# Kernel optimization log

Hardware: AMD Instinct MI355X
Metric: run time of the kernel (lower is better)

Reference implementation:

```python
import jax, jax.numpy as jnp
import numpy as np

B, S, HID = 2, 2048, 2048
H, DN, DR, KVR, DV = 16, 128, 64, 512, 128
THETA = 10000.0
EPS = 1e-6
SCALE = (DN + DR) ** -0.5  # softmax_scale = q_head_dim ** -0.5 (rope_scaling is None)


def setup_inputs() -> dict:
    key = jax.random.key(0)
    ks = jax.random.split(key, 8)
    std = 0.02
    return {
        "hidden_states": jax.random.normal(ks[0], (B, S, HID), jnp.float32),
        "q_nope_weight": jax.random.normal(ks[1], (H * DN, HID), jnp.float32) * std,
        "q_pe_weight": jax.random.normal(ks[2], (H * DR, HID), jnp.float32) * std,
        "kv_a_weight": jax.random.normal(ks[3], (KVR + DR, HID), jnp.float32) * std,
        "kv_a_ln_weight": jnp.ones((KVR,), jnp.float32),
        "k_b_weight": jax.random.normal(ks[4], (H, DN, KVR), jnp.float32) * std,
        "v_b_weight": jax.random.normal(ks[5], (H, DV, KVR), jnp.float32) * std,
        "o_weight": jax.random.normal(ks[6], (HID, H * DV), jnp.float32) * std,
        "position_ids": jnp.arange(S, dtype=jnp.int32)[None, :],
    }


def _rotate_half(x):
    x1, x2 = jnp.split(x, 2, axis=-1)
    return jnp.concatenate((-x2, x1), axis=-1)


def _interleave(x):
    # torch: x.view(..., d//2, 2).transpose(-1, -2).reshape(..., d)
    *lead, d = x.shape
    x = x.reshape(*lead, d // 2, 2)
    x = jnp.swapaxes(x, -1, -2)
    return x.reshape(*lead, d)


def reference(hidden_states, q_nope_weight, q_pe_weight, kv_a_weight,
              kv_a_ln_weight, k_b_weight, v_b_weight, o_weight, position_ids):
    b, s, _ = hidden_states.shape
    # Q projections, split into no-rope and rope parts per head
    q_nope = jnp.einsum('bsh,ndh->bnsd', hidden_states, q_nope_weight.reshape(H, DN, HID))
    q_pe = jnp.einsum('bsh,ndh->bnsd', hidden_states, q_pe_weight.reshape(H, DR, HID))
    # Joint low-rank KV + shared rope-key projection (MQA-style)
    ckv_kpe = jnp.einsum('bsh,ch->bsc', hidden_states, kv_a_weight)  # [b,s,KVR+DR]
    ckv, k_pe = ckv_kpe[..., :KVR], ckv_kpe[..., KVR:]
    # RMSNorm over the compressed latent (kv_a_layernorm)
    var = jnp.mean(jnp.square(ckv), axis=-1, keepdims=True)
    ckv = ckv * jax.lax.rsqrt(var + EPS) * kv_a_ln_weight  # [b,s,KVR]
    # Rotary tables: cos/sin indexed by position_ids, broadcast over heads
    inv_freq = 1.0 / (THETA ** (jnp.arange(0, DR, 2, dtype=jnp.float32) / DR))
    t = position_ids.astype(jnp.float32)                 # [1,s]
    freqs = t[..., None] * inv_freq                      # [1,s,DR/2]
    emb = jnp.concatenate((freqs, freqs), axis=-1)       # [1,s,DR]
    cos = jnp.cos(emb)[:, None]                          # [1,1,s,DR]
    sin = jnp.sin(emb)[:, None]
    # Partial RoPE with the interleave permutation from apply_rotary_pos_emb
    q_pe = _interleave(q_pe)
    k_pe = _interleave(k_pe[:, None])                    # [b,1,s,DR]
    q_pe = q_pe * cos + _rotate_half(q_pe) * sin
    k_pe = (k_pe * cos + _rotate_half(k_pe) * sin)[:, 0] # [b,s,DR]
    # Weight absorption: fold k_b into q, attend directly in the latent space
    q_lat = jnp.einsum('bnsd,ndc->bnsc', q_nope, k_b_weight)  # [b,H,s,KVR]
    scores = (jnp.einsum('bnsc,btc->bnst', q_lat, ckv)
              + jnp.einsum('bnsd,btd->bnst', q_pe, k_pe)) * SCALE
    mask = jnp.tril(jnp.ones((s, s), dtype=bool))
    scores = jnp.where(mask, scores, jnp.finfo(scores.dtype).min)
    attn = jax.nn.softmax(scores, axis=-1)
    # Attention output in the latent space, then expand with v_b and o_proj
    out_lat = jnp.einsum('bnst,btc->bnsc', attn, ckv)         # [b,H,s,KVR]
    v_out = jnp.einsum('bnsc,ndc->bnsd', out_lat, v_b_weight) # [b,H,s,DV]
    v_out = v_out.transpose(0, 2, 1, 3).reshape(b, s, H * DV)
    return jnp.einsum('bsf,hf->bsh', v_out, o_weight)
```

## Files before the change

### kernel.cpp

```cpp
#include <hip/hip_runtime.h>
#include <hip/hip_bf16.h>


typedef __hip_bfloat16 bf16;
typedef __bf16 v8bf __attribute__((ext_vector_type(8)));
typedef float  v4f  __attribute__((ext_vector_type(4)));

#define S_    2048
#define SCALE_F 0.07216878364870322f

__device__ __forceinline__ void st1(float* p, float v){ *p = v; }
__device__ __forceinline__ void st1(bf16* p, float v){ *p = __float2bfloat16(v); }
__device__ __forceinline__ unsigned short bfb(float x){
  return __builtin_bit_cast(unsigned short, __float2bfloat16(x));
}
__device__ __forceinline__ unsigned pk2(float a, float b){
  return (unsigned)bfb(a) | ((unsigned)bfb(b) << 16);
}

typedef const void __attribute__((address_space(1)))* gas_t;
typedef void __attribute__((address_space(3)))* las_t;
__device__ __forceinline__ void g2l16(const void* g, void* l){
  __builtin_amdgcn_global_load_lds((gas_t)g, (las_t)l, 16, 0, 0);
}

__global__ void cossin_kernel(const int* __restrict__ pos, float* __restrict__ cosT,
                              float* __restrict__ sinT){
  int idx = blockIdx.x*256 + threadIdx.x;
  int i = idx & 31, s = idx >> 5;
  float t = (float)pos[s];
  float freq = t * powf(10000.0f, -(float)i/32.0f);
  cosT[idx] = cosf(freq);
  sinT[idx] = sinf(freq);
}

__global__ void castf2b_kernel(const float* __restrict__ src, bf16* __restrict__ dst, int n8){
  int i = blockIdx.x*256 + threadIdx.x;
  if (i >= n8) return;
  const float4* s = (const float4*)src;
  float4 a = s[2*i], b = s[2*i+1];
  uint4 o; o.x = pk2(a.x,a.y); o.y = pk2(a.z,a.w); o.z = pk2(b.x,b.y); o.w = pk2(b.z,b.w);
  ((uint4*)dst)[i] = o;
}

template<typename TC>
__global__ __launch_bounds__(256) void gemm2_kernel(
    const bf16* __restrict__ A, int lda, int aDiv, long aS1, long aS2,
    const bf16* __restrict__ W, int ldw, int wDiv, long wS1, long wS2,
    TC* __restrict__ C, int ldc, int cDiv, long cS1, long cS2,
    int N, int K, float alpha)
{
  int z = blockIdx.z;
  A += (long)(z/aDiv)*aS1 + (long)(z%aDiv)*aS2;
  W += (long)(z/wDiv)*wS1 + (long)(z%wDiv)*wS2;
  C += (long)(z/cDiv)*cS1 + (long)(z%cDiv)*cS2;
  __shared__ bf16 As[2][4096];
  __shared__ bf16 Ws[2][4096];
  const int tid = threadIdx.x;
  const int w = tid>>6, l = tid&63, g = l>>4, c16 = l&15;
  const int wr = (w>>1)*64, wc = (w&1)*64;
  const int row0 = blockIdx.y*128, col0 = blockIdx.x*128;

  const long aO1 = (long)(row0 + (tid>>2))*lda + (tid&3)*8;
  const long aO2 = (long)(row0 + 64 + (tid>>2))*lda + (tid&3)*8;
  int wr1 = col0 + (tid>>2);      if (wr1 > N-1) wr1 = N-1;
  int wr2 = col0 + 64 + (tid>>2); if (wr2 > N-1) wr2 = N-1;
  const long wO1 = (long)wr1*ldw + (tid&3)*8;
  const long wO2 = (long)wr2*ldw + (tid&3)*8;

  v4f acc[4][4];
  #pragma unroll
  for (int i=0;i<4;i++)
    #pragma unroll
    for (int j=0;j<4;j++) acc[i][j] = (v4f){0.f,0.f,0.f,0.f};

  auto STAGE = [&](int k0, int bsel){
    g2l16(A + aO1 + k0, &As[bsel][tid*8]);
    g2l16(A + aO2 + k0, &As[bsel][2048 + tid*8]);
    g2l16(W + wO1 + k0, &Ws[bsel][tid*8]);
    g2l16(W + wO2 + k0, &Ws[bsel][2048 + tid*8]);
  };
  STAGE(0, 0);
  __syncthreads();
  const int nk = K >> 5;
  for (int t=0; t<nk; ++t){
    const int cur = t & 1;
    if (t+1 < nk) STAGE((t+1)*32, cur^1);
    v8bf af[4], bw[4];
    #pragma unroll
    for (int mi=0;mi<4;mi++) af[mi] = *(const v8bf*)&As[cur][(wr+mi*16+c16)*32 + g*8];
    #pragma unroll
    for (int ni=0;ni<4;ni++) bw[ni] = *(const v8bf*)&Ws[cur][(wc+ni*16+c16)*32 + g*8];
    #pragma unroll
    for (int mi=0;mi<4;mi++)
      #pragma unroll
      for (int ni=0;ni<4;ni++)
        acc[mi][ni] = __builtin_amdgcn_mfma_f32_16x16x32_bf16(af[mi], bw[ni], acc[mi][ni], 0,0,0);
    __syncthreads();
  }
  #pragma unroll
  for (int mi=0;mi<4;mi++)
    #pragma unroll
    for (int ni=0;ni<4;ni++)
      #pragma unroll
      for (int r=0;r<4;r++){
        int row = row0 + wr + mi*16 + g*4 + r;
        int col = col0 + wc + ni*16 + c16;
        if (col < N) st1(C + (long)row*ldc + col, acc[mi][ni][r]*alpha);
      }
}

__global__ __launch_bounds__(256) void proj3_kernel(
    const bf16* __restrict__ A,
    const bf16* __restrict__ Wq, const bf16* __restrict__ Wp, const bf16* __restrict__ Wc,
    bf16* __restrict__ Cq, bf16* __restrict__ Cp, bf16* __restrict__ Cc)
{
  const int bx = blockIdx.x;
  const bf16* W; bf16* C; int ldc, N, col0;
  if (bx < 16){ W = Wq; C = Cq; ldc = 2048; N = 2048; col0 = bx*128; }
  else if (bx < 24){ W = Wp; C = Cp; ldc = 1024; N = 1024; col0 = (bx-16)*128; }
  else { W = Wc; C = Cc; ldc = 576; N = 576; col0 = (bx-24)*128; }
  __shared__ bf16 As[2][4096];
  __shared__ bf16 Ws[2][4096];
  const int tid = threadIdx.x;
  const int w = tid>>6, l = tid&63, g = l>>4, c16 = l&15;
  const int wr = (w>>1)*64, wc = (w&1)*64;
  const int row0 = blockIdx.y*128;

  const long aO1 = (long)(row0 + (tid>>2))*2048 + (tid&3)*8;
  const long aO2 = (long)(row0 + 64 + (tid>>2))*2048 + (tid&3)*8;
  int wr1 = col0 + (tid>>2);      if (wr1 > N-1) wr1 = N-1;
  int wr2 = col0 + 64 + (tid>>2); if (wr2 > N-1) wr2 = N-1;
  const long wO1 = (long)wr1*2048 + (tid&3)*8;
  const long wO2 = (long)wr2*2048 + (tid&3)*8;

  v4f acc[4][4];
  #pragma unroll
  for (int i=0;i<4;i++)
    #pragma unroll
    for (int j=0;j<4;j++) acc[i][j] = (v4f){0.f,0.f,0.f,0.f};

  auto STAGE = [&](int k0, int bsel){
    g2l16(A + aO1 + k0, &As[bsel][tid*8]);
    g2l16(A + aO2 + k0, &As[bsel][2048 + tid*8]);
    g2l16(W + wO1 + k0, &Ws[bsel][tid*8]);
    g2l16(W + wO2 + k0, &Ws[bsel][2048 + tid*8]);
  };
  STAGE(0, 0);
  __syncthreads();
  for (int t=0; t<64; ++t){
    const int cur = t & 1;
    if (t+1 < 64) STAGE((t+1)*32, cur^1);
    v8bf af[4], bw[4];
    #pragma unroll
    for (int mi=0;mi<4;mi++) af[mi] = *(const v8bf*)&As[cur][(wr+mi*16+c16)*32 + g*8];
    #pragma unroll
    for (int ni=0;ni<4;ni++) bw[ni] = *(const v8bf*)&Ws[cur][(wc+ni*16+c16)*32 + g*8];
    #pragma unroll
    for (int mi=0;mi<4;mi++)
      #pragma unroll
      for (int ni=0;ni<4;ni++)
        acc[mi][ni] = __builtin_amdgcn_mfma_f32_16x16x32_bf16(af[mi], bw[ni], acc[mi][ni], 0,0,0);
    __syncthreads();
  }
  #pragma unroll
  for (int mi=0;mi<4;mi++)
    #pragma unroll
    for (int ni=0;ni<4;ni++)
      #pragma unroll
      for (int r=0;r<4;r++){
        int row = row0 + wr + mi*16 + g*4 + r;
        int col = col0 + wc + ni*16 + c16;
        if (col < N) C[(long)row*ldc + col] = __float2bfloat16(acc[mi][ni][r]);
      }
}

__global__ __launch_bounds__(256) void kbT_kernel(const float* __restrict__ kb,
                                                  bf16* __restrict__ kbT){
  __shared__ bf16 t[64][65];
  int h = blockIdx.z, c0 = blockIdx.x*64, d0 = blockIdx.y*64;
  const float* src = kb + ((long)h*128 + d0)*512 + c0;
  #pragma unroll
  for (int i=0;i<16;i++){
    int idx = i*256 + threadIdx.x;
    int dl = idx>>6, cl = idx&63;
    t[dl][cl] = __float2bfloat16(src[(long)dl*512 + cl]);
  }
  __syncthreads();
  bf16* dst = kbT + ((long)h*512 + c0)*128 + d0;
  #pragma unroll
  for (int i=0;i<16;i++){
    int idx = i*256 + threadIdx.x;
    int cl = idx>>6, dl = idx&63;
    dst[(long)cl*128 + dl] = t[dl][cl];
  }
}

__global__ __launch_bounds__(256) void tposeV_kernel(const bf16* __restrict__ Kb,
                                                     bf16* __restrict__ Kd){
  __shared__ bf16 t[64][65];
  int b = blockIdx.z, s0 = blockIdx.y*64, d0 = blockIdx.x*64;
  const bf16* src = Kb + ((long)(b*S_ + s0))*576 + d0;
  #pragma unroll
  for (int i=0;i<16;i++){
    int idx = i*256 + threadIdx.x;
    int sl = idx>>6, dl = idx&63;
    t[sl][dl] = src[(long)sl*576 + dl];
  }
  __syncthreads();
  bf16* dst = Kd + ((long)(b*512 + d0))*S_ + s0;
  #pragma unroll
  for (int i=0;i<16;i++){
    int idx = i*256 + threadIdx.x;
    int dl = idx>>6, sl = idx&63;
    dst[(long)dl*S_ + sl] = t[sl][dl];
  }
}

__global__ __launch_bounds__(256) void build_k_kernel(
    const bf16* __restrict__ ckv_kpe, const float* __restrict__ ln_w,
    const float* __restrict__ cosT, const float* __restrict__ sinT,
    bf16* __restrict__ Kb)
{
  int row = blockIdx.x;
  int s = row & (S_-1);
  int tid = threadIdx.x;
  const bf16* src = ckv_kpe + (long)row*576;
  float x0 = __bfloat162float(src[tid*2]), x1 = __bfloat162float(src[tid*2+1]);
  float ss = x0*x0 + x1*x1;
  #pragma unroll
  for (int o=32;o>=1;o>>=1) ss += __shfl_xor(ss, o, 64);
  __shared__ float wss[4];
  int wid = tid>>6, lane = tid&63;
  if (lane==0) wss[wid] = ss;
  __syncthreads();
  float tot = wss[0]+wss[1]+wss[2]+wss[3];
  float rs = rsqrtf(tot*(1.0f/512.0f) + 1e-6f);
  bf16* dst = Kb + (long)row*576;
  dst[tid*2]   = __float2bfloat16(x0*rs*ln_w[tid*2]);
  dst[tid*2+1] = __float2bfloat16(x1*rs*ln_w[tid*2+1]);
  if (tid < 32) {
    float p0 = __bfloat162float(src[512 + tid*2]);
    float p1 = __bfloat162float(src[512 + tid*2 + 1]);
    float c = cosT[s*32+tid], sn = sinT[s*32+tid];
    dst[512+tid] = __float2bfloat16(p0*c - p1*sn);
    dst[544+tid] = __float2bfloat16(p1*c + p0*sn);
  }
}

__global__ void rope_q_kernel(const bf16* __restrict__ qpe,
                              const float* __restrict__ cosT, const float* __restrict__ sinT,
                              bf16* __restrict__ Qb)
{
  int idx = blockIdx.x*256 + threadIdx.x;
  int i = idx & 31;
  int s = (idx >> 5) & (S_-1);
  int z = idx >> 16;
  int b = z >> 4, n = z & 15;
  long base = ((long)(b*S_+s))*1024 + n*64 + 2*i;
  float x0 = __bfloat162float(qpe[base]), x1 = __bfloat162float(qpe[base+1]);
  float c = cosT[s*32+i], sn = sinT[s*32+i];
  bf16* dst = Qb + ((long)z*S_ + s)*576;
  dst[512+i] = __float2bfloat16((x0*c - x1*sn)*SCALE_F);
  dst[544+i] = __float2bfloat16((x1*c + x0*sn)*SCALE_F);
}

#define K0_OFF 0
#define K1_OFF 36864
#define V0_OFF 73728
#define V1_OFF 106496
#define SX_OFF 139264
#define P_OFF  147456
#define SMEM_BYTES 152576

__global__ __launch_bounds__(512, 2) void attn_mfma_kernel(
    const bf16* __restrict__ Qg, const bf16* __restrict__ Kg,
    const bf16* __restrict__ Vdg, bf16* __restrict__ Og)
{
  extern __shared__ char smem[];
  const int tid = threadIdx.x;
  const int w   = tid >> 6;
  const int l   = tid & 63;
  const int g   = l >> 4;
  const int c16 = l & 15;
  const int rg  = w & 3;
  const int dh  = w >> 2;
  const int R   = rg * 16;
  const int Dh  = dh * 256;
  const int DQb = dh * 576;
  char* SX = smem + SX_OFF + rg*2048;
  char* Pp = smem + P_OFF  + rg*1280;

  const int lin = blockIdx.x;
  const int k8 = lin & 7;
  const int b  = k8 >> 2;
  const int u  = (lin >> 3)*4 + (k8 & 3);
  const int n  = u & 15;
  const int pr = u >> 4;
  const int z  = b*16 + n;

  const char* kb0 = (const char*)Kg  + (long)b*S_*1152;
  const char* vd0 = (const char*)Vdg + (long)b*512*S_*2;

  int kOffG[5], kOffL[5], vOffG[4], vOffL[4];
  #pragma unroll
  for (int it=0; it<4; it++){
    int c = it*512 + tid;
    int kcol = c/72, j = c - kcol*72;
    kOffG[it] = kcol*1152 + ((j ^ (kcol&7))<<4);
    kOffL[it] = c*16;
  }
  {
    int c = 2048 + tid;
    int kcol = c/72, j = c - kcol*72;
    kOffG[4] = kcol*1152 + ((j ^ (kcol&7))<<4);
    kOffL[4] = c*16;
  }
  #pragma unroll
  for (int it=0; it<4; it++){
    int c = it*512 + tid;
    int s = c>>3, uu = (c&7) ^ (s&7);
    int d = 2*s + (uu>>2), j = uu&3;
    vOffG[it] = d*(S_*2) + j*16;
    vOffL[it] = c*16;
  }

  auto STAGE = [&](int tt, char* kd, char* vd){
    const char* ksrc = kb0 + (long)tt*36864;
    #pragma unroll
    for (int it=0; it<4; it++) g2l16(ksrc + kOffG[it], kd + kOffL[it]);
    if (tid < 256) g2l16(ksrc + kOffG[4], kd + kOffL[4]);
    const char* vsrc = vd0 + (long)tt*64;
    #pragma unroll
    for (int it=0; it<4; it++) g2l16(vsrc + vOffG[it], vd + vOffL[it]);
  };

  for (int ph = 0; ph < 2; ++ph){
    const int qt = ph ? (31 - pr) : pr;
    const int q0 = qt * 64;

    v8bf qf[9];
    {
      const char* qgb = (const char*)Qg + ((long)z*S_ + q0 + R + c16)*1152 + DQb;
      #pragma unroll
      for (int kk=0;kk<9;kk++) qf[kk] = *(const v8bf*)(qgb + kk*64 + g*16);
    }
    v4f acc[16];
    #pragma unroll
    for (int i=0;i<16;i++) acc[i] = (v4f){0.f,0.f,0.f,0.f};
    float m2[2] = {-1e30f,-1e30f};
    float lsum[4] = {0.f,0.f,0.f,0.f};

    const int ntile = 2*qt + 2;
    __syncthreads();
    STAGE(0, smem + K0_OFF, smem + V0_OFF);

    for (int t = 0; t < ntile; ++t){
      asm volatile("s_waitcnt vmcnt(0)" ::: "memory");
      __syncthreads();
      char* kB = smem + ((t&1) ? K1_OFF : K0_OFF);
      char* vB = smem + ((t&1) ? V1_OFF : V0_OFF);
      if (t+1 < ntile)
        STAGE(t+1, smem + (((t+1)&1) ? K1_OFF : K0_OFF),
                    smem + (((t+1)&1) ? V1_OFF : V0_OFF));

      v4f s0 = (v4f){0.f,0.f,0.f,0.f}, s1 = (v4f){0.f,0.f,0.f,0.f};
      #pragma unroll
      for (int kk=0;kk<9;kk++){
        int j = dh*36 + kk*4 + g;
        v8bf kf0 = *(const v8bf*)(kB + c16*1152      + ((j ^ (c16&7))<<4));
        v8bf kf1 = *(const v8bf*)(kB + (16+c16)*1152 + ((j ^ (c16&7))<<4));
        s0 = __builtin_amdgcn_mfma_f32_16x16x32_bf16(qf[kk], kf0, s0, 0,0,0);
        s1 = __builtin_amdgcn_mfma_f32_16x16x32_bf16(qf[kk], kf1, s1, 0,0,0);
      }
      {
        const int pr0 = 2*(1-dh);
        #pragma unroll
        for (int rr=0; rr<2; rr++){
          int r = pr0 + rr;
          int row = g*4 + r;
          *(float*)(SX + row*128 + (((c16      + 4*row)&31)<<2)) = s0[r];
          *(float*)(SX + row*128 + (((16 + c16 + 4*row)&31)<<2)) = s1[r];
        }
      }
      asm volatile("s_waitcnt lgkmcnt(0)" ::: "memory");
      __builtin_amdgcn_s_barrier();
      __builtin_amdgcn_sched_barrier(0);
      {
        const int or0 = 2*dh;
        #pragma unroll
        for (int rr=0; rr<2; rr++){
          int r = or0 + rr;
          int row = g*4 + r;
          float v0 = s0[r] + *(const float*)(SX + row*128 + (((c16      + 4*row)&31)<<2));
          float v1 = s1[r] + *(const float*)(SX + row*128 + (((16 + c16 + 4*row)&31)<<2));
          if (t >= ntile-2){
            int kt0 = t*32;
            int qrow = q0 + R + row;
            if (kt0 + c16 > qrow)      v0 = -1e30f;
            if (kt0 + 16 + c16 > qrow) v1 = -1e30f;
          }
          float pm = fmaxf(v0, v1);
          pm = fmaxf(pm, __shfl_xor(pm, 1)); pm = fmaxf(pm, __shfl_xor(pm, 2));
          pm = fmaxf(pm, __shfl_xor(pm, 4)); pm = fmaxf(pm, __shfl_xor(pm, 8));
          float alv = 1.0f;
          if (pm > m2[rr] + 8.0f){
            alv = __expf(m2[rr] - pm);
            m2[rr] = pm;
          }
          float p0 = __expf(v0 - m2[rr]);
          float p1 = __expf(v1 - m2[rr]);
          int bse = (row>>1)*128;
          int sw  = (row>>1)&7;
          *(unsigned short*)(Pp + bse + (((((row&1)<<2)|(c16>>3)) ^ sw)<<4) + (c16&7)*2) = bfb(p0);
          *(unsigned short*)(Pp + bse + (((((row&1)<<2)|(2+(c16>>3))) ^ sw)<<4) + (c16&7)*2) = bfb(p1);
          float sv = p0 + p1;
          sv += __shfl_xor(sv, 1); sv += __shfl_xor(sv, 2);
          sv += __shfl_xor(sv, 4); sv += __shfl_xor(sv, 8);
          if (c16 == 0) *(float2*)(Pp + 1024 + row*8) = make_float2(alv, sv);
        }
      }
      asm volatile("s_waitcnt lgkmcnt(0)" ::: "memory");
      __builtin_amdgcn_s_barrier();
      __builtin_amdgcn_sched_barrier(0);
      {
        float ax[4];
        #pragma unroll
        for (int r=0;r<4;r++){
          float2 ap = *(const float2*)(Pp + 1024 + (g*4+r)*8);
          lsum[r] = lsum[r]*ap.x + ap.y;
          ax[r] = ap.x;
        }
        if (ax[0]!=1.0f || ax[1]!=1.0f || ax[2]!=1.0f || ax[3]!=1.0f){
          #pragma unroll
          for (int cb=0;cb<16;cb++)
            #pragma unroll
            for (int r=0;r<4;r++) acc[cb][r] *= ax[r];
        }
        int prow = c16;
        int au = ((((prow&1)<<2)) | g) ^ ((prow>>1)&7);
        v8bf af = *(const v8bf*)(Pp + (prow>>1)*128 + (au<<4));
        #pragma unroll
        for (int cb=0;cb<16;cb++){
          int d = Dh + cb*16 + c16;
          int vu = ((((d&1)<<2)) | g) ^ ((d>>1)&7);
          v8bf vf = *(const v8bf*)(vB + (d>>1)*128 + (vu<<4));
          acc[cb] = __builtin_amdgcn_mfma_f32_16x16x32_bf16(af, vf, acc[cb], 0,0,0);
        }
      }
    }
    float inv[4];
    #pragma unroll
    for (int r=0;r<4;r++) inv[r] = 1.0f / lsum[r];
    #pragma unroll
    for (int cb=0;cb<16;cb++)
      #pragma unroll
      for (int r=0;r<4;r++){
        int qrow = q0 + R + g*4 + r;
        Og[((long)z*S_ + qrow)*512 + Dh + cb*16 + c16] = __float2bfloat16(acc[cb][r]*inv[r]);
      }
  }
}

extern "C" void kernel_launch(void* const* d_in, const int* in_sizes, int n_in,
                              void* d_out, int out_size, void* d_ws, size_t ws_size,
                              hipStream_t stream)
{
  const float* hidden = (const float*)d_in[0];
  const float* qn_w   = (const float*)d_in[1];
  const float* qpe_w  = (const float*)d_in[2];
  const float* kva_w  = (const float*)d_in[3];
  const float* ln_w   = (const float*)d_in[4];
  const float* kb_w   = (const float*)d_in[5];
  const float* vb_w   = (const float*)d_in[6];
  const float* o_w    = (const float*)d_in[7];
  const int*   pos    = (const int*)d_in[8];
  float* out = (float*)d_out;
  char* ws = (char*)d_ws;

  float* cosT  = (float*)(ws);
  float* sinT  = (float*)(ws + 262144);
  bf16*  ckvb  = (bf16*) (ws + 524288);
  bf16*  vbb   = (bf16*) (ws + 524288);
  bf16*  Qb    = (bf16*) (ws + 5242880);
  bf16*  ob    = (bf16*) (ws + 5242880);
  bf16*  Kb    = (bf16*) (ws + 80740352);
  bf16*  outl  = (bf16*) (ws + 85458944);
  bf16*  qnopeb= (bf16*) (ws + 85458944);
  bf16*  qpeb  = (bf16*) (ws + 102236160);
  bf16*  kbT   = (bf16*) (ws + 110624768);
  bf16*  hb    = (bf16*) (ws + 112721920);
  bf16*  qnb   = (bf16*) (ws + 129499136);
  bf16*  qpw   = (bf16*) (ws + 137887744);
  bf16*  kvab  = (bf16*) (ws + 142082048);
  bf16*  voutb = (bf16*) (ws + 152567808);
  bf16*  Kd    = (bf16*) (ws + 169345024);

  static_assert(sizeof(v8bf) == 16, "v8bf must be 16B");
  hipFuncSetAttribute((const void*)attn_mfma_kernel,
                      hipFuncAttributeMaxDynamicSharedMemorySize, SMEM_BYTES);

  cossin_kernel<<<256, 256, 0, stream>>>(pos, cosT, sinT);

  castf2b_kernel<<<4096, 256, 0, stream>>>(hidden, hb, 1048576);
  castf2b_kernel<<<2048, 256, 0, stream>>>(qn_w,  qnb, 524288);
  castf2b_kernel<<<1024, 256, 0, stream>>>(qpe_w, qpw, 262144);
  castf2b_kernel<<< 576, 256, 0, stream>>>(kva_w, kvab, 147456);

  proj3_kernel<<<dim3(29,32,1),256,0,stream>>>(hb, qnb, qpw, kvab,
                                               qnopeb, qpeb, ckvb);

  kbT_kernel<<<dim3(8,2,16), 256, 0, stream>>>(kb_w, kbT);
  build_k_kernel<<<4096, 256, 0, stream>>>(ckvb, ln_w, cosT, sinT, Kb);
  castf2b_kernel<<<512, 256, 0, stream>>>(vb_w, vbb, 131072);
  tposeV_kernel<<<dim3(8,32,2), 256, 0, stream>>>(Kb, Kd);
  rope_q_kernel<<<8192, 256, 0, stream>>>(qpeb, cosT, sinT, Qb);

  gemm2_kernel<bf16><<<dim3(4,16,32),256,0,stream>>>(
      qnopeb,2048, 16,(long)S_*2048,128,  kbT,128, 16,0,65536,
      Qb,576, 1,(long)S_*576,0,  512,128, SCALE_F);

  attn_mfma_kernel<<<dim3(512), 512, SMEM_BYTES, stream>>>(Qb, Kb, Kd, outl);

  castf2b_kernel<<<2048, 256, 0, stream>>>(o_w, ob, 524288);

  gemm2_kernel<bf16><<<dim3(1,16,32),256,0,stream>>>(
      outl,512, 1,(long)S_*512,0,  vbb,512, 16,0,65536,
      voutb,2048, 16,(long)S_*2048,128,  128,512, 1.f);

  gemm2_kernel<float><<<dim3(16,32,1),256,0,stream>>>(
      voutb,2048, 1,0,0,  ob,2048, 1,0,0,  out,2048, 1,0,0,  2048,2048, 1.f);
}
```

Before: 601.5 us.

## Transpose QK MFMA and redistribute P via shuffles to drop a barrier

Measured after the change: 550.9 us. 1.09x faster.

```diff
diff --git a/kernel.cpp b/kernel.cpp
--- a/kernel.cpp
+++ b/kernel.cpp
@@ -5,6 +5,7 @@
 typedef __hip_bfloat16 bf16;
 typedef __bf16 v8bf __attribute__((ext_vector_type(8)));
 typedef float  v4f  __attribute__((ext_vector_type(4)));
+typedef unsigned int v4u __attribute__((ext_vector_type(4)));
 
 #define S_    2048
 #define SCALE_F 0.07216878364870322f
@@ -270,8 +271,7 @@
 #define V0_OFF 73728
 #define V1_OFF 106496
 #define SX_OFF 139264
-#define P_OFF  147456
-#define SMEM_BYTES 152576
+#define SMEM_BYTES 155648
 
 __global__ __launch_bounds__(512, 2) void attn_mfma_kernel(
     const bf16* __restrict__ Qg, const bf16* __restrict__ Kg,
@@ -288,8 +288,8 @@
   const int R   = rg * 16;
   const int Dh  = dh * 256;
   const int DQb = dh * 576;
-  char* SX = smem + SX_OFF + rg*2048;
-  char* Pp = smem + P_OFF  + rg*1280;
+  char* SXw = smem + SX_OFF + rg*4096 + dh*2048;
+  char* SXr = smem + SX_OFF + rg*4096 + (1-dh)*2048;
 
   const int lin = blockIdx.x;
   const int k8 = lin & 7;
@@ -335,6 +335,13 @@
     for (int it=0; it<4; it++) g2l16(vsrc + vOffG[it], vd + vOffL[it]);
   };
 
+  int sxo[4];
+  #pragma unroll
+  for (int r=0;r<4;r++) sxo[r] = c16*128 + ((((g*4+r) + c16) & 15)<<3);
+  const int srcA = ((2*g)&3)*16 + c16;
+  const int srcB = ((2*g+1)&3)*16 + c16;
+  const bool hiG = (g >= 2);
+
   for (int ph = 0; ph < 2; ++ph){
     const int qt = ph ? (31 - pr) : pr;
     const int q0 = qt * 64;
@@ -348,8 +355,8 @@
     v4f acc[16];
     #pragma unroll
     for (int i=0;i<16;i++) acc[i] = (v4f){0.f,0.f,0.f,0.f};
-    float m2[2] = {-1e30f,-1e30f};
-    float lsum[4] = {0.f,0.f,0.f,0.f};
+    float mL = -1e30f;
+    float lsumL = 0.f;
 
     const int ntile = 2*qt + 2;
     __syncthreads();
@@ -370,94 +377,83 @@
         int j = dh*36 + kk*4 + g;
         v8bf kf0 = *(const v8bf*)(kB + c16*1152      + ((j ^ (c16&7))<<4));
         v8bf kf1 = *(const v8bf*)(kB + (16+c16)*1152 + ((j ^ (c16&7))<<4));
-        s0 = __builtin_amdgcn_mfma_f32_16x16x32_bf16(qf[kk], kf0, s0, 0,0,0);
-        s1 = __builtin_amdgcn_mfma_f32_16x16x32_bf16(qf[kk], kf1, s1, 0,0,0);
-      }
-      {
-        const int pr0 = 2*(1-dh);
-        #pragma unroll
-        for (int rr=0; rr<2; rr++){
-          int r = pr0 + rr;
-          int row = g*4 + r;
-          *(float*)(SX + row*128 + (((c16      + 4*row)&31)<<2)) = s0[r];
-          *(float*)(SX + row*128 + (((16 + c16 + 4*row)&31)<<2)) = s1[r];
-        }
-      }
+        s0 = __builtin_amdgcn_mfma_f32_16x16x32_bf16(kf0, qf[kk], s0, 0,0,0);
+        s1 = __builtin_amdgcn_mfma_f32_16x16x32_bf16(kf1, qf[kk], s1, 0,0,0);
+      }
+      #pragma unroll
+      for (int r=0;r<4;r++)
+        *(float2*)(SXw + sxo[r]) = make_float2(s0[r], s1[r]);
       asm volatile("s_waitcnt lgkmcnt(0)" ::: "memory");
       __builtin_amdgcn_s_barrier();
       __builtin_amdgcn_sched_barrier(0);
-      {
-        const int or0 = 2*dh;
-        #pragma unroll
-        for (int rr=0; rr<2; rr++){
-          int r = or0 + rr;
-          int row = g*4 + r;
-          float v0 = s0[r] + *(const float*)(SX + row*128 + (((c16      + 4*row)&31)<<2));
-          float v1 = s1[r] + *(const float*)(SX + row*128 + (((16 + c16 + 4*row)&31)<<2));
-          if (t >= ntile-2){
-            int kt0 = t*32;
-            int qrow = q0 + R + row;
-            if (kt0 + c16 > qrow)      v0 = -1e30f;
-            if (kt0 + 16 + c16 > qrow) v1 = -1e30f;
-          }
-          float pm = fmaxf(v0, v1);
-          pm = fmaxf(pm, __shfl_xor(pm, 1)); pm = fmaxf(pm, __shfl_xor(pm, 2));
-          pm = fmaxf(pm, __shfl_xor(pm, 4)); pm = fmaxf(pm, __shfl_xor(pm, 8));
-          float alv = 1.0f;
-          if (pm > m2[rr] + 8.0f){
-            alv = __expf(m2[rr] - pm);
-            m2[rr] = pm;
-          }
-          float p0 = __expf(v0 - m2[rr]);
-          float p1 = __expf(v1 - m2[rr]);
-          int bse = (row>>1)*128;
-          int sw  = (row>>1)&7;
-          *(unsigned short*)(Pp + bse + (((((row&1)<<2)|(c16>>3)) ^ sw)<<4) + (c16&7)*2) = bfb(p0);
-          *(unsigned short*)(Pp + bse + (((((row&1)<<2)|(2+(c16>>3))) ^ sw)<<4) + (c16&7)*2) = bfb(p1);
-          float sv = p0 + p1;
-          sv += __shfl_xor(sv, 1); sv += __shfl_xor(sv, 2);
-          sv += __shfl_xor(sv, 4); sv += __shfl_xor(sv, 8);
-          if (c16 == 0) *(float2*)(Pp + 1024 + row*8) = make_float2(alv, sv);
-        }
-      }
-      asm volatile("s_waitcnt lgkmcnt(0)" ::: "memory");
-      __builtin_amdgcn_s_barrier();
-      __builtin_amdgcn_sched_barrier(0);
-      {
-        float ax[4];
+      #pragma unroll
+      for (int r=0;r<4;r++){
+        float2 o = *(const float2*)(SXr + sxo[r]);
+        s0[r] += o.x; s1[r] += o.y;
+      }
+      if (t >= ntile-2){
+        int kt0 = t*32;
+        int qrow = q0 + R + c16;
         #pragma unroll
         for (int r=0;r<4;r++){
-          float2 ap = *(const float2*)(Pp + 1024 + (g*4+r)*8);
-          lsum[r] = lsum[r]*ap.x + ap.y;
-          ax[r] = ap.x;
+          if (kt0 + g*4 + r > qrow)      s0[r] = -1e30f;
+          if (kt0 + 16 + g*4 + r > qrow) s1[r] = -1e30f;
         }
-        if (ax[0]!=1.0f || ax[1]!=1.0f || ax[2]!=1.0f || ax[3]!=1.0f){
+      }
+      float pm = fmaxf(fmaxf(fmaxf(s0[0],s0[1]),fmaxf(s0[2],s0[3])),
+                       fmaxf(fmaxf(s1[0],s1[1]),fmaxf(s1[2],s1[3])));
+      pm = fmaxf(pm, __shfl_xor(pm, 16));
+      pm = fmaxf(pm, __shfl_xor(pm, 32));
+      float alv = 1.0f;
+      if (pm > mL + 8.0f){ alv = __expf(mL - pm); mL = pm; }
+      float p0[4], p1[4];
+      float sv = 0.f;
+      #pragma unroll
+      for (int r=0;r<4;r++){
+        p0[r] = __expf(s0[r] - mL);
+        p1[r] = __expf(s1[r] - mL);
+        sv += p0[r] + p1[r];
+      }
+      sv += __shfl_xor(sv, 16);
+      sv += __shfl_xor(sv, 32);
+      lsumL = lsumL*alv + sv;
+      unsigned u0 = pk2(p0[0],p0[1]), u1 = pk2(p0[2],p0[3]);
+      unsigned u2 = pk2(p1[0],p1[1]), u3 = pk2(p1[2],p1[3]);
+      unsigned a0 = __shfl(u0, srcA), a1 = __shfl(u1, srcA);
+      unsigned a2 = __shfl(u2, srcA), a3 = __shfl(u3, srcA);
+      unsigned b0 = __shfl(u0, srcB), b1 = __shfl(u1, srcB);
+      unsigned b2 = __shfl(u2, srcB), b3 = __shfl(u3, srcB);
+      v4u paw;
+      paw.x = hiG ? a2 : a0;  paw.y = hiG ? a3 : a1;
+      paw.z = hiG ? b2 : b0;  paw.w = hiG ? b3 : b1;
+      v8bf pa = __builtin_bit_cast(v8bf, paw);
+      if (!__all((int)(alv == 1.0f))){
+        float alr[4];
+        #pragma unroll
+        for (int r=0;r<4;r++) alr[r] = __shfl(alv, (l & 48) | (g*4+r));
+        #pragma unroll
+        for (int cb=0;cb<16;cb++)
           #pragma unroll
-          for (int cb=0;cb<16;cb++)
-            #pragma unroll
-            for (int r=0;r<4;r++) acc[cb][r] *= ax[r];
-        }
-        int prow = c16;
-        int au = ((((prow&1)<<2)) | g) ^ ((prow>>1)&7);
-        v8bf af = *(const v8bf*)(Pp + (prow>>1)*128 + (au<<4));
-        #pragma unroll
-        for (int cb=0;cb<16;cb++){
-          int d = Dh + cb*16 + c16;
-          int vu = ((((d&1)<<2)) | g) ^ ((d>>1)&7);
-          v8bf vf = *(const v8bf*)(vB + (d>>1)*128 + (vu<<4));
-          acc[cb] = __builtin_amdgcn_mfma_f32_16x16x32_bf16(af, vf, acc[cb], 0,0,0);
-        }
+          for (int r=0;r<4;r++) acc[cb][r] *= alr[r];
+      }
+      #pragma unroll
+      for (int cb=0;cb<16;cb++){
+        int d = Dh + cb*16 + c16;
+        int vu = ((((d&1)<<2)) | g) ^ ((d>>1)&7);
+        v8bf vf = *(const v8bf*)(vB + (d>>1)*128 + (vu<<4));
+        acc[cb] = __builtin_amdgcn_mfma_f32_16x16x32_bf16(pa, vf, acc[cb], 0,0,0);
       }
     }
-    float inv[4];
-    #pragma unroll
-    for (int r=0;r<4;r++) inv[r] = 1.0f / lsum[r];
+    float invL = 1.0f / lsumL;
+    float invr[4];
+    #pragma unroll
+    for (int r=0;r<4;r++) invr[r] = __shfl(invL, (l & 48) | (g*4+r));
     #pragma unroll
     for (int cb=0;cb<16;cb++)
       #pragma unroll
       for (int r=0;r<4;r++){
         int qrow = q0 + R + g*4 + r;
-        Og[((long)z*S_ + qrow)*512 + Dh + cb*16 + c16] = __float2bfloat16(acc[cb][r]*inv[r]);
+        Og[((long)z*S_ + qrow)*512 + Dh + cb*16 + c16] = __float2bfloat16(acc[cb][r]*invr[r]);
       }
   }
 }
```
